# Performance work log

Measured on AMD Instinct MI355X. Metric: run time of the kernel, lower is better.

The kernel has to match this reference:

```python
import jax, jax.numpy as jnp
import numpy as np

VIEW_NUM = 360
CHAN_NUM = 512
BATCH = 2
IMG = 512


def setup_inputs() -> dict:
    key = jax.random.key(0)
    x = jax.random.normal(key, (BATCH, 1, IMG, IMG), dtype=jnp.float32)
    return {"x": x}


def _bilinear_sample_zeros(img, ix, iy):
    """Bilinear sample img (B,1,H,W) at pixel coords ix, iy (H,W), zeros padding.
    Matches F.grid_sample(mode='bilinear', padding_mode='zeros', align_corners=False)."""
    H, W = img.shape[-2], img.shape[-1]
    x0 = jnp.floor(ix)
    y0 = jnp.floor(iy)
    x1 = x0 + 1.0
    y1 = y0 + 1.0
    wx1 = ix - x0
    wx0 = 1.0 - wx1
    wy1 = iy - y0
    wy0 = 1.0 - wy1

    def gather(yy, xx):
        valid = (xx >= 0) & (xx <= W - 1) & (yy >= 0) & (yy <= H - 1)
        xi = jnp.clip(xx, 0, W - 1).astype(jnp.int32)
        yi = jnp.clip(yy, 0, H - 1).astype(jnp.int32)
        # fancy-index over spatial dims -> (B,1,H,W)
        return img[:, :, yi, xi] * valid.astype(img.dtype)

    return (gather(y0, x0) * (wy0 * wx0)
            + gather(y0, x1) * (wy0 * wx1)
            + gather(y1, x0) * (wy1 * wx0)
            + gather(y1, x1) * (wy1 * wx1))


def _fp(x):
    B, C, H, W = x.shape
    # affine_grid base coords, align_corners=False: (2i+1)/N - 1
    bx = (2.0 * jnp.arange(W, dtype=x.dtype) + 1.0) / W - 1.0
    by = (2.0 * jnp.arange(H, dtype=x.dtype) + 1.0) / H - 1.0
    X = bx[None, :]  # (1,W)
    Y = by[:, None]  # (H,1)
    i = jnp.arange(VIEW_NUM, dtype=x.dtype)
    angles = -jnp.pi * (i + 1.0) / VIEW_NUM - jnp.pi
    cosv = jnp.cos(angles)
    sinv = jnp.sin(angles)

    def per_view(carry, cs):
        c, s = cs
        # theta = [[c,-s,0],[s,c,0]]; grid = base @ theta^T
        gx = c * X - s * Y  # (H,W) normalized sample x
        gy = s * X + c * Y  # (H,W) normalized sample y
        # unnormalize (align_corners=False)
        ix = ((gx + 1.0) * W - 1.0) * 0.5
        iy = ((gy + 1.0) * H - 1.0) * 0.5
        samp = _bilinear_sample_zeros(x, ix, iy)  # (B,1,H,W)
        return carry, jnp.sum(samp, axis=2)  # sum over height -> (B,1,W)

    _, cols = jax.lax.scan(per_view, 0, (cosv, sinv))  # (V,B,1,W)
    sino = jnp.transpose(cols, (1, 2, 3, 0)) * 0.5  # (B,1,chanNum,viewNum)
    return sino


def reference(x):
    return _fp(x)
```

## Files before the change

### kernel.cpp

```cpp
#include <hip/hip_runtime.h>

typedef __fp16 h2 __attribute__((ext_vector_type(2)));

constexpr int VIEWS = 360;
constexpr int IMGSZ = 512;
constexpr int WCHUNK = 64;
constexpr int KH = 64;
constexpr int PITCH = 101;
constexpr int MAXNY = 94;
constexpr int LDSDW = PITCH * MAXNY;
constexpr int PW = 712;
constexpr int PH = 704;
constexpr int PAD = 96;

__global__ __launch_bounds__(256) void pad_kernel(const float* __restrict__ x,
                                                  unsigned* __restrict__ padq) {
    constexpr int PW4 = PW / 4;
    constexpr int total = PH * PW4;
    int idx = blockIdx.x * 256 + threadIdx.x;
    if (idx >= total) return;
    int py = idx / PW4;
    int px4 = idx - py * PW4;
    int gx = px4 * 4 - PAD;
    int gy = py - PAD;
    const float* img0 = x;
    const float* img1 = x + (size_t)IMGSZ * IMGSZ;
    float4 a = make_float4(0.f, 0.f, 0.f, 0.f);
    float4 bq = a;
    if ((unsigned)gy < (unsigned)IMGSZ && (unsigned)gx < (unsigned)IMGSZ) {
        size_t off = (size_t)gy * IMGSZ + gx;
        a  = *(const float4*)(img0 + off);
        bq = *(const float4*)(img1 + off);
    }
    uint4 d;
    d.x = __builtin_bit_cast(unsigned, __builtin_amdgcn_cvt_pkrtz(a.x, bq.x));
    d.y = __builtin_bit_cast(unsigned, __builtin_amdgcn_cvt_pkrtz(a.y, bq.y));
    d.z = __builtin_bit_cast(unsigned, __builtin_amdgcn_cvt_pkrtz(a.z, bq.z));
    d.w = __builtin_bit_cast(unsigned, __builtin_amdgcn_cvt_pkrtz(a.w, bq.w));
    *(uint4*)&padq[(size_t)idx * 4] = d;
}

__global__ __launch_bounds__(256, 4) void fp_kernel(const unsigned* __restrict__ padq,
                                                    float* __restrict__ out) {
    __shared__ __align__(16) unsigned tileU[LDSDW];

    int blk = blockIdx.x;
    int wc = blk & 7;
    int v = blk >> 3;

    int tid = threadIdx.x;
    int lane = tid & 63;
    int g = tid >> 6;
    int w = wc * WCHUNK + lane;

    int r = tid & 127;
    int b = tid >> 7;

    double ang = -3.14159265358979323846 * (double)(v + 1) / (double)VIEWS
                 - 3.14159265358979323846;
    float c = (float)cos(ang);
    float s = (float)sin(ang);

    float xw = (float)w + 0.5f - 256.0f;
    float cxw = fmaf(c, xw, 255.5f);
    float sxw = fmaf(s, xw, 255.5f);

    float lo = -1e30f, hi = 1e30f;
    {
        float coef = -s, base = cxw;
        if (fabsf(coef) > 1e-6f) {
            float a = (-1.0f - base) / coef;
            float bq = (512.0f - base) / coef;
            lo = fmaxf(lo, fminf(a, bq));
            hi = fminf(hi, fmaxf(a, bq));
        } else if (!(base > -1.0f && base < 512.0f)) {
            lo = 1e30f; hi = -1e30f;
        }
    }
    {
        float coef = c, base = sxw;
        if (fabsf(coef) > 1e-6f) {
            float a = (-1.0f - base) / coef;
            float bq = (512.0f - base) / coef;
            lo = fmaxf(lo, fminf(a, bq));
            hi = fminf(hi, fmaxf(a, bq));
        } else if (!(base > -1.0f && base < 512.0f)) {
            lo = 1e30f; hi = -1e30f;
        }
    }
    float h0f = fminf(fmaxf(floorf(lo + 255.5f) - 1.0f, 0.0f), 512.0f);
    float h1f = fminf(fmaxf(ceilf(hi + 255.5f) + 1.0f, -1.0f), 511.0f);
    int h0 = (int)h0f;
    int h1 = (int)h1f;

    int bh0 = h0, bh1 = h1;
    #pragma unroll
    for (int m = 1; m < 64; m <<= 1) {
        bh0 = min(bh0, __shfl_xor(bh0, m, 64));
        bh1 = max(bh1, __shfl_xor(bh1, m, 64));
    }

    float xa = (float)(wc * WCHUNK) + 0.5f - 256.0f;
    float xb = xa + 63.0f;

    float acc0 = 0.0f, acc1 = 0.0f;
    float step4x = -4.0f * s;
    float step4y = 4.0f * c;

    for (int hc = bh0; hc <= bh1; hc += KH) {
        int hend = min(hc + KH - 1, bh1);

        float ha = (float)hc - 255.5f;
        float hb = (float)hend - 255.5f;
        float ix00 = c * xa - s * ha, ix01 = c * xa - s * hb;
        float ix10 = c * xb - s * ha, ix11 = c * xb - s * hb;
        float iy00 = s * xa + c * ha, iy01 = s * xa + c * hb;
        float iy10 = s * xb + c * ha, iy11 = s * xb + c * hb;
        float ixmn = fminf(fminf(ix00, ix01), fminf(ix10, ix11)) + 255.5f;
        float iymn = fminf(fminf(iy00, iy01), fminf(iy10, iy11)) + 255.5f;
        float iymx = fmaxf(fmaxf(iy00, iy01), fmaxf(iy10, iy11)) + 255.5f;
        int x_lo = (int)floorf(ixmn) - 1;
        int x_lo4 = x_lo & ~3;
        int y_lo = (int)floorf(iymn) - 1;
        int NY = min((int)floorf(iymx) + 3 - y_lo, MAXNY);

        __syncthreads();

        if (r < NY) {
            const unsigned* src = padq + (y_lo + PAD + r) * PW
                                       + (x_lo4 + PAD) + (b << 2);
            int dst = r * PITCH + (b << 2);
            uint4 cur = *(const uint4*)src;
            #pragma unroll
            for (int it = 0; it < 12; ++it) {
                uint4 nxt;
                if (it < 11 || b == 0)
                    nxt = *(const uint4*)(src + 8 * (it + 1));
                int d = dst + (it << 3);
                tileU[d]     = cur.x;
                tileU[d + 1] = cur.y;
                tileU[d + 2] = cur.z;
                tileU[d + 3] = cur.w;
                cur = nxt;
            }
            if (b == 0) {
                int d = dst + (12 << 3);
                tileU[d]     = cur.x;
                tileU[d + 1] = cur.y;
                tileU[d + 2] = cur.z;
                tileU[d + 3] = cur.w;
            }
        }
        __syncthreads();

        float hh0 = (float)(hc + g) - 255.5f;
        float ixr = fmaf(-s, hh0, cxw) - (float)x_lo4;
        float iyr = fmaf(c, hh0, sxw) - (float)y_lo;
        h2 accp0 = (h2)0.0f;
        h2 accp1 = (h2)0.0f;
        int parity = 0;
        #pragma unroll 8
        for (int h = hc + g; h <= hend; h += 4) {
            float tx = truncf(ixr);
            float ty = truncf(iyr);
            float wx1 = ixr - tx;
            float wy1 = iyr - ty;
            h2 wxs = __builtin_amdgcn_cvt_pkrtz(wx1, wx1);
            h2 wys = __builtin_amdgcn_cvt_pkrtz(wy1, wy1);
            unsigned a = (unsigned)fmaf(ty, 404.0f, tx * 4.0f);
            const unsigned* p = (const unsigned*)((const char*)tileU + a);
            h2 t00 = __builtin_bit_cast(h2, p[0]);
            h2 t01 = __builtin_bit_cast(h2, p[1]);
            h2 t10 = __builtin_bit_cast(h2, p[PITCH]);
            h2 t11 = __builtin_bit_cast(h2, p[PITCH + 1]);
            h2 r0 = t00 + (t01 - t00) * wxs;
            h2 r1 = t10 + (t11 - t10) * wxs;
            h2 contrib = r0 + (r1 - r0) * wys;
            if (parity) accp1 += contrib; else accp0 += contrib;
            parity ^= 1;
            ixr += step4x;
            iyr += step4y;
        }
        acc0 += (float)accp0.x + (float)accp1.x;
        acc1 += (float)accp0.y + (float)accp1.y;
    }

    __syncthreads();
    tileU[(g << 6) + lane] = __float_as_uint(acc0);
    tileU[256 + (g << 6) + lane] = __float_as_uint(acc1);
    __syncthreads();
    if (g == 0) {
        float r0 = __uint_as_float(tileU[lane]) + __uint_as_float(tileU[64 + lane]) +
                   __uint_as_float(tileU[128 + lane]) + __uint_as_float(tileU[192 + lane]);
        float r1 = __uint_as_float(tileU[256 + lane]) + __uint_as_float(tileU[320 + lane]) +
                   __uint_as_float(tileU[384 + lane]) + __uint_as_float(tileU[448 + lane]);
        size_t o = (size_t)w * VIEWS + v;
        out[o] = r0 * 0.5f;
        out[(size_t)IMGSZ * VIEWS + o] = r1 * 0.5f;
    }
}

extern "C" void kernel_launch(void* const* d_in, const int* in_sizes, int n_in,
                              void* d_out, int out_size, void* d_ws, size_t ws_size,
                              hipStream_t stream) {
    const float* x = (const float*)d_in[0];
    float* out = (float*)d_out;
    unsigned* padq = (unsigned*)d_ws;

    constexpr int padTotal = PH * (PW / 4);
    pad_kernel<<<(padTotal + 255) / 256, 256, 0, stream>>>(x, padq);

    int nblocks = VIEWS * (IMGSZ / WCHUNK);
    fp_kernel<<<nblocks, 256, 0, stream>>>(padq, out);
}
```

Before: 155.4 us.

## Double block size to 512 threads and flatten tile load across all threads

Raises the projection block from 256 to 512 threads, so 8 wavefronts split the height rows of each chunk instead of 4, each stepping by 8 rows. The LDS tile fill becomes a flat strided loop over all tile uint4 elements, replacing the per-row loader that used only 2*NY threads. The final reduction sums 8 partials and writes both batch outputs from two wavefronts. This shortens each thread's serial inner loop and spreads load work evenly, at the cost of more integer division in the fill and more partial sums to combine.

```diff
diff --git a/kernel.cpp b/kernel.cpp
--- a/kernel.cpp
+++ b/kernel.cpp
@@ -12,6 +12,7 @@
 constexpr int PW = 712;
 constexpr int PH = 704;
 constexpr int PAD = 96;
+constexpr int NT = 512;
 
 __global__ __launch_bounds__(256) void pad_kernel(const float* __restrict__ x,
                                                   unsigned* __restrict__ padq) {
@@ -40,8 +41,8 @@
     *(uint4*)&padq[(size_t)idx * 4] = d;
 }
 
-__global__ __launch_bounds__(256, 4) void fp_kernel(const unsigned* __restrict__ padq,
-                                                    float* __restrict__ out) {
+__global__ __launch_bounds__(NT, 8) void fp_kernel(const unsigned* __restrict__ padq,
+                                                   float* __restrict__ out) {
     __shared__ __align__(16) unsigned tileU[LDSDW];
 
     int blk = blockIdx.x;
@@ -50,11 +51,8 @@
 
     int tid = threadIdx.x;
     int lane = tid & 63;
-    int g = tid >> 6;
+    int p = tid >> 6;
     int w = wc * WCHUNK + lane;
-
-    int r = tid & 127;
-    int b = tid >> 7;
 
     double ang = -3.14159265358979323846 * (double)(v + 1) / (double)VIEWS
                  - 3.14159265358979323846;
@@ -104,8 +102,8 @@
     float xb = xa + 63.0f;
 
     float acc0 = 0.0f, acc1 = 0.0f;
-    float step4x = -4.0f * s;
-    float step4y = 4.0f * c;
+    float step8x = -8.0f * s;
+    float step8y = 8.0f * c;
 
     for (int hc = bh0; hc <= bh1; hc += KH) {
         int hend = min(hc + KH - 1, bh1);
@@ -123,44 +121,34 @@
         int x_lo4 = x_lo & ~3;
         int y_lo = (int)floorf(iymn) - 1;
         int NY = min((int)floorf(iymx) + 3 - y_lo, MAXNY);
+        int total4 = NY * 25;
+        int nit = (total4 + NT - 1) >> 9;
 
         __syncthreads();
 
-        if (r < NY) {
-            const unsigned* src = padq + (y_lo + PAD + r) * PW
-                                       + (x_lo4 + PAD) + (b << 2);
-            int dst = r * PITCH + (b << 2);
-            uint4 cur = *(const uint4*)src;
-            #pragma unroll
-            for (int it = 0; it < 12; ++it) {
-                uint4 nxt;
-                if (it < 11 || b == 0)
-                    nxt = *(const uint4*)(src + 8 * (it + 1));
-                int d = dst + (it << 3);
-                tileU[d]     = cur.x;
-                tileU[d + 1] = cur.y;
-                tileU[d + 2] = cur.z;
-                tileU[d + 3] = cur.w;
-                cur = nxt;
+        {
+            const unsigned* pb = padq + (y_lo + PAD) * PW + (x_lo4 + PAD);
+            for (int k = 0; k < nit; ++k) {
+                int ic = min((k << 9) + tid, total4 - 1);
+                int ry = ic / 25;
+                uint4 val = *(const uint4*)(pb + 4 * ic + (PW - 100) * ry);
+                int d = (ic << 2) + ry;
+                tileU[d]     = val.x;
+                tileU[d + 1] = val.y;
+                tileU[d + 2] = val.z;
+                tileU[d + 3] = val.w;
             }
-            if (b == 0) {
-                int d = dst + (12 << 3);
-                tileU[d]     = cur.x;
-                tileU[d + 1] = cur.y;
-                tileU[d + 2] = cur.z;
-                tileU[d + 3] = cur.w;
-            }
         }
         __syncthreads();
 
-        float hh0 = (float)(hc + g) - 255.5f;
+        float hh0 = (float)(hc + p) - 255.5f;
         float ixr = fmaf(-s, hh0, cxw) - (float)x_lo4;
         float iyr = fmaf(c, hh0, sxw) - (float)y_lo;
         h2 accp0 = (h2)0.0f;
         h2 accp1 = (h2)0.0f;
         int parity = 0;
         #pragma unroll 8
-        for (int h = hc + g; h <= hend; h += 4) {
+        for (int h = hc + p; h <= hend; h += 8) {
             float tx = truncf(ixr);
             float ty = truncf(iyr);
             float wx1 = ixr - tx;
@@ -168,35 +156,34 @@
             h2 wxs = __builtin_amdgcn_cvt_pkrtz(wx1, wx1);
             h2 wys = __builtin_amdgcn_cvt_pkrtz(wy1, wy1);
             unsigned a = (unsigned)fmaf(ty, 404.0f, tx * 4.0f);
-            const unsigned* p = (const unsigned*)((const char*)tileU + a);
-            h2 t00 = __builtin_bit_cast(h2, p[0]);
-            h2 t01 = __builtin_bit_cast(h2, p[1]);
-            h2 t10 = __builtin_bit_cast(h2, p[PITCH]);
-            h2 t11 = __builtin_bit_cast(h2, p[PITCH + 1]);
+            const unsigned* pt = (const unsigned*)((const char*)tileU + a);
+            h2 t00 = __builtin_bit_cast(h2, pt[0]);
+            h2 t01 = __builtin_bit_cast(h2, pt[1]);
+            h2 t10 = __builtin_bit_cast(h2, pt[PITCH]);
+            h2 t11 = __builtin_bit_cast(h2, pt[PITCH + 1]);
             h2 r0 = t00 + (t01 - t00) * wxs;
             h2 r1 = t10 + (t11 - t10) * wxs;
             h2 contrib = r0 + (r1 - r0) * wys;
             if (parity) accp1 += contrib; else accp0 += contrib;
             parity ^= 1;
-            ixr += step4x;
-            iyr += step4y;
+            ixr += step8x;
+            iyr += step8y;
         }
         acc0 += (float)accp0.x + (float)accp1.x;
         acc1 += (float)accp0.y + (float)accp1.y;
     }
 
     __syncthreads();
-    tileU[(g << 6) + lane] = __float_as_uint(acc0);
-    tileU[256 + (g << 6) + lane] = __float_as_uint(acc1);
+    tileU[(p << 6) + lane] = __float_as_uint(acc0);
+    tileU[512 + (p << 6) + lane] = __float_as_uint(acc1);
     __syncthreads();
-    if (g == 0) {
-        float r0 = __uint_as_float(tileU[lane]) + __uint_as_float(tileU[64 + lane]) +
-                   __uint_as_float(tileU[128 + lane]) + __uint_as_float(tileU[192 + lane]);
-        float r1 = __uint_as_float(tileU[256 + lane]) + __uint_as_float(tileU[320 + lane]) +
-                   __uint_as_float(tileU[384 + lane]) + __uint_as_float(tileU[448 + lane]);
+    if (p < 2) {
+        const unsigned* base = tileU + (p << 9);
+        float r = 0.0f;
+        #pragma unroll
+        for (int q = 0; q < 8; ++q) r += __uint_as_float(base[(q << 6) + lane]);
         size_t o = (size_t)w * VIEWS + v;
-        out[o] = r0 * 0.5f;
-        out[(size_t)IMGSZ * VIEWS + o] = r1 * 0.5f;
+        out[o + (size_t)p * IMGSZ * VIEWS] = r * 0.5f;
     }
 }
 
@@ -211,5 +198,5 @@
     pad_kernel<<<(padTotal + 255) / 256, 256, 0, stream>>>(x, padq);
 
     int nblocks = VIEWS * (IMGSZ / WCHUNK);
-    fp_kernel<<<nblocks, 256, 0, stream>>>(padq, out);
+    fp_kernel<<<nblocks, NT, 0, stream>>>(padq, out);
 }
```

New measurement: 171.6 us. 1.1x slower.
